# Performance work log

Hardware: AMD Instinct MI355X
Metric: run time of the kernel (lower is better)

## Reference

```python
import jax, jax.numpy as jnp
import numpy as np

B, C, H, W, NCH = 2, 256, 48, 48, 12


def setup_inputs() -> dict:
    key = jax.random.key(0)
    k1, k2, k3, k4, k5 = jax.random.split(key, 5)
    gray_feature = jax.random.normal(k1, (B, C, H, W), jnp.float32)
    rgb_feature = jax.random.normal(k2, (B, C, H, W), jnp.float32)
    rgb_image = jax.random.uniform(k3, (B, 3, H, W), jnp.float32)
    # one-hot segmentation labels: random class id per pixel in [0, NCH)
    gcls = jax.random.randint(k4, (B, H, W), 0, NCH)
    rcls = jax.random.randint(k5, (B, H, W), 0, NCH)
    gray_label = jax.nn.one_hot(gcls, NCH, axis=1, dtype=jnp.float32)
    rgb_label = jax.nn.one_hot(rcls, NCH, axis=1, dtype=jnp.float32)
    return dict(gray_feature=gray_feature, rgb_feature=rgb_feature,
                rgb_image=rgb_image, gray_label=gray_label, rgb_label=rgb_label)


def _masked_normalize(feat, maskf):
    # feat: [b,c,N], maskf: [b,N] in {0,1}. Subtract per-channel masked mean,
    # then divide each masked pixel's feature vector by its channel-norm.
    cnt = maskf.sum(-1)                                            # [b]
    mean = jnp.einsum('bcn,bn->bc', feat, maskf) / jnp.maximum(cnt, 1.0)[:, None]
    bar = (feat - mean[:, :, None]) * maskf[:, None, :]            # zero outside mask
    norm = jnp.sqrt(jnp.sum(bar * bar, axis=1))                    # [b,N]
    unit = bar / jnp.where(norm > 0, norm, 1.0)[:, None, :]
    return unit, cnt


def reference(gray_feature, rgb_feature, rgb_image, gray_label, rgb_label):
    b, c, h, w = gray_feature.shape
    N = h * w
    gf = gray_feature.reshape(b, c, N)
    rf = rgb_feature.reshape(b, c, N)
    img = rgb_image.reshape(b, 3, N)
    gms = gray_label.reshape(b, -1, N) > 0.5   # [b,NCH,N] bool
    rms = rgb_label.reshape(b, -1, N) > 0.5
    canvas = -jnp.ones((b, 3, N), gray_feature.dtype)
    NEG = jnp.asarray(-1e30, gray_feature.dtype)
    for k in range(1, 12):  # classes 1..11, matching the torch loop
        gm = gms[:, k]                                     # [b,N]
        rm = rms[:, k]
        gmf = gm.astype(gf.dtype)
        rmf = rm.astype(rf.dtype)
        gn, cg = _masked_normalize(gf, gmf)                # [b,c,N]
        rn, cr = _masked_normalize(rf, rmf)
        # normalized correlation between gray and rgb masked pixels
        corr = jnp.einsum('bci,bcj->bij', gn, rn)          # [b,N,N]
        logits = jnp.where(rm[:, None, :], corr, NEG)      # softmax over rgb-mask pixels
        sm = jax.nn.softmax(logits, axis=-1)
        out = jnp.einsum('bij,bcj->bci', sm, img)          # [b,3,N]
        # skip condition from torch: needs >=2 pixels on each side
        valid = (cg > 1) & (cr > 1)                        # [b]
        write = gm & valid[:, None]                        # [b,N]
        canvas = jnp.where(write[:, None, :], out, canvas)
    return canvas.reshape(b, 3, h, w)
```

## Files before the change

### kernel.cpp

```cpp
#include <hip/hip_runtime.h>
#include <math.h>

#define BN 2
#define CC 256
#define NN 2304
#define KK 12
#define MC 320
#define QT 16
#define KTL 256
#define KCH 32
#define BPAD 260
#define APAD 18
#define KB_ACT 11

#define OFF_CNT_G   0
#define OFF_CNT_R   32
#define OFF_IDX_G   64
#define OFF_CPS_G   (OFF_IDX_G + BN * KK * MC)
#define OFF_CPS_R   (OFF_CPS_G + BN * NN)
#define OFF_MSUM_G  (OFF_CPS_R + BN * NN)
#define OFF_MSUM_R  (OFF_MSUM_G + BN * KK * CC)
#define OFF_IMGC    (OFF_MSUM_R + BN * KK * CC)
#define OFF_INV_G   (OFF_IMGC + BN * KK * 3 * MC)
#define OFF_INV_R   (OFF_INV_G + BN * KK * MC)
#define OFF_UCG     (OFF_INV_R + BN * KK * MC)
#define OFF_UCR     (OFF_UCG + BN * KK * MC * CC)

__global__ __launch_bounds__(256) void prep_mean_kernel(
        const float* __restrict__ gf, const float* __restrict__ rf,
        const float* __restrict__ img, const float* __restrict__ gl,
        const float* __restrict__ rl, float* __restrict__ out,
        int* cnt_g, int* cnt_r, int* idx_g, int* cps_g, int* cps_r,
        float* imgc, float* inv_g, float* inv_r,
        float* msum_g, float* msum_r) {
    __shared__ int wcnt[4];
    __shared__ float wsum[4][4][KK];
    int bid = blockIdx.x, tid = threadIdx.x;
    int lane = tid & 63, wid = tid >> 6;

    if (bid < 48) {
        int type = bid / (BN * KK);
        int rem = bid % (BN * KK);
        int b = rem / KK, k = rem % KK;
        const float* lp = (type ? rl : gl) + ((size_t)(b * KK + k)) * NN;
        int* cps = type ? cps_r : cps_g;
        int* cnt = type ? cnt_r : cnt_g;
        int base = 0;
        for (int c0 = 0; c0 < NN; c0 += 256) {
            int i = c0 + tid;
            bool p = lp[i] > 0.5f;
            unsigned long long m = __ballot(p);
            int rank = __popcll(m & ((1ull << lane) - 1));
            if (lane == 0) wcnt[wid] = __popcll(m);
            __syncthreads();
            int pre = 0;
            for (int w = 0; w < wid; ++w) pre += wcnt[w];
            int tot = wcnt[0] + wcnt[1] + wcnt[2] + wcnt[3];
            if (p) {
                int pos = base + pre + rank;
                cps[b * NN + i] = (k << 16) | pos;
                if (pos < MC) {
                    if (type) {
                        for (int ch = 0; ch < 3; ++ch)
                            imgc[((b * KK + k) * 3 + ch) * MC + pos] =
                                img[((size_t)(b * 3 + ch)) * NN + i];
                    } else {
                        idx_g[(b * KK + k) * MC + pos] = i;
                    }
                }
            }
            base += tot;
            __syncthreads();
        }
        if (tid == 0) cnt[b * KK + k] = base;
        int start = base < MC ? base : MC;
        for (int pos = start + tid; pos < MC; pos += 256) {
            if (type) {
                for (int ch = 0; ch < 3; ++ch)
                    imgc[((b * KK + k) * 3 + ch) * MC + pos] = 0.f;
            } else {
                idx_g[(b * KK + k) * MC + pos] = 0;
            }
        }
        float* invc = type ? inv_r : inv_g;
        for (int pos = tid; pos < MC; pos += 256)
            invc[(b * KK + k) * MC + pos] = 0.f;
    } else {
        int u = bid - 48;
        if (u < 54) out[u * 256 + tid] = -1.0f;
        int type = u >> 7;
        int rem = u & 127;
        int b = rem >> 6, cg = rem & 63;
        const float* fb = (type ? rf : gf) + ((size_t)(b * CC + cg * 4)) * NN;
        const float* lab = (type ? rl : gl) + ((size_t)b) * KK * NN;
        float* msum = type ? msum_r : msum_g;

        float acc[4][KK];
        #pragma unroll
        for (int c = 0; c < 4; ++c)
            #pragma unroll
            for (int kk = 0; kk < KK; ++kk) acc[c][kk] = 0.f;
        for (int i = tid; i < NN; i += 256) {
            float lv[KK];
            #pragma unroll
            for (int kk = 0; kk < KK; ++kk) lv[kk] = lab[(size_t)kk * NN + i];
            #pragma unroll
            for (int c = 0; c < 4; ++c) {
                float v = fb[(size_t)c * NN + i];
                #pragma unroll
                for (int kk = 0; kk < KK; ++kk) acc[c][kk] += lv[kk] * v;
            }
        }
        #pragma unroll
        for (int c = 0; c < 4; ++c)
            #pragma unroll
            for (int kk = 0; kk < KK; ++kk) {
                #pragma unroll
                for (int o = 32; o; o >>= 1)
                    acc[c][kk] += __shfl_xor(acc[c][kk], o, 64);
            }
        if (lane == 0) {
            #pragma unroll
            for (int c = 0; c < 4; ++c)
                #pragma unroll
                for (int kk = 0; kk < KK; ++kk) wsum[wid][c][kk] = acc[c][kk];
        }
        __syncthreads();
        if (tid < 48) {
            int c = tid / KK, kk = tid % KK;
            float s = wsum[0][c][kk] + wsum[1][c][kk] + wsum[2][c][kk] + wsum[3][c][kk];
            msum[(b * KK + kk) * CC + cg * 4 + c] = s;
        }
    }
}

__global__ __launch_bounds__(256) void center_kernel(
        const float* __restrict__ gf, const float* __restrict__ rf,
        const int* __restrict__ cps_g, const int* __restrict__ cps_r,
        const int* __restrict__ cnt_g, const int* __restrict__ cnt_r,
        const float* __restrict__ msum_g, const float* __restrict__ msum_r,
        float* ucg, float* ucr, float* inv_g, float* inv_r) {
    const int PCH = NN / 32;
    int blk = blockIdx.x;
    int type = blk / (BN * PCH);
    int rem = blk % (BN * PCH);
    int b = rem / PCH, chunk = rem % PCH;
    int i0 = chunk * 32;
    const float* f = type ? rf : gf;
    const int* cps = type ? cps_r : cps_g;
    const int* cnt = type ? cnt_r : cnt_g;
    const float* msum = type ? msum_r : msum_g;
    float* uc = type ? ucr : ucg;
    float* invc = type ? inv_r : inv_g;

    __shared__ float lmean[KK * 257];
    __shared__ float tile[64 * 33];

    int tid = threadIdx.x;
    int pl = tid & 31, cb = tid >> 5;

    float r[8];
    #pragma unroll
    for (int j = 0; j < 8; ++j)
        r[j] = f[((size_t)(b * CC + cb * 8 + j)) * NN + i0 + pl];

    for (int x = tid; x < KK * CC; x += 256) {
        int k = x >> 8, c = x & 255;
        float cn = fmaxf((float)cnt[b * KK + k], 1.f);
        lmean[k * 257 + c] = msum[(b * KK + k) * CC + c] / cn;
    }
    int p = tid >> 3, q = tid & 7;
    int kcpos = cps[b * NN + i0 + p];
    int kc = kcpos >> 16, pos = kcpos & 0xFFFF;
    bool wr = pos < MC;
    float ss = 0.f;
    float* ub = uc + ((size_t)((b * KK + kc) * MC + (wr ? pos : MC - 1))) * CC;
    for (int cc = 0; cc < 4; ++cc) {
        __syncthreads();
        #pragma unroll
        for (int j = 0; j < 8; ++j)
            tile[(cb * 8 + j) * 33 + pl] = r[j];
        if (cc < 3) {
            #pragma unroll
            for (int j = 0; j < 8; ++j)
                r[j] = f[((size_t)(b * CC + (cc + 1) * 64 + cb * 8 + j)) * NN + i0 + pl];
        }
        __syncthreads();
        #pragma unroll
        for (int h = 0; h < 2; ++h) {
            int c0 = q * 8 + h * 4;
            float4 v;
            v.x = tile[(c0 + 0) * 33 + p] - lmean[kc * 257 + cc * 64 + c0 + 0];
            v.y = tile[(c0 + 1) * 33 + p] - lmean[kc * 257 + cc * 64 + c0 + 1];
            v.z = tile[(c0 + 2) * 33 + p] - lmean[kc * 257 + cc * 64 + c0 + 2];
            v.w = tile[(c0 + 3) * 33 + p] - lmean[kc * 257 + cc * 64 + c0 + 3];
            ss += v.x * v.x + v.y * v.y + v.z * v.z + v.w * v.w;
            if (wr) *(float4*)&ub[cc * 64 + c0] = v;
        }
    }
    ss += __shfl_xor(ss, 1, 64);
    ss += __shfl_xor(ss, 2, 64);
    ss += __shfl_xor(ss, 4, 64);
    if (q == 0 && wr)
        invc[(b * KK + kc) * MC + pos] = (ss > 0.f) ? rsqrtf(ss) : 1.0f;
}

__global__ __launch_bounds__(512) void corr_out_kernel(
        const int* __restrict__ cnt_g, const int* __restrict__ cnt_r,
        const int* __restrict__ idx_g,
        const float* __restrict__ ucg, const float* __restrict__ ucr,
        const float* __restrict__ inv_g, const float* __restrict__ inv_r,
        const float* __restrict__ imgc, float* __restrict__ out) {
    const int TNQ = MC / QT;
    const int NWG = BN * KB_ACT * TNQ;
    int bid = blockIdx.x;
    int x = (bid & 7) * (NWG / 8) + (bid >> 3);
    int tq = x % TNQ;
    int rest = x / TNQ;
    int k = 1 + rest % KB_ACT;
    int b = rest / KB_ACT;
    int bk = b * KK + k;
    int cg_ = cnt_g[bk], cr_ = cnt_r[bk];
    if (cg_ <= 1 || cr_ <= 1) return;
    int Mg = min(cg_, MC), Mr = min(cr_, MC);
    int q0 = tq * QT;
    if (q0 >= Mg) return;
    int mrp = (Mr + 3) & ~3;

    __shared__ float Af[CC * APAD];
    __shared__ float Bs[KCH * BPAD];

    int tid = threadIdx.x;
    {
        int r = tid >> 5, c32 = tid & 31;
        int rowi = q0 + r; if (rowi > MC - 1) rowi = MC - 1;
        const float* rowA = ucg + ((size_t)(bk * MC + rowi)) * CC;
        float4 v0 = *(const float4*)&rowA[c32 * 8];
        float4 v1 = *(const float4*)&rowA[c32 * 8 + 4];
        Af[(c32 * 8 + 0) * APAD + r] = v0.x;
        Af[(c32 * 8 + 1) * APAD + r] = v0.y;
        Af[(c32 * 8 + 2) * APAD + r] = v0.z;
        Af[(c32 * 8 + 3) * APAD + r] = v0.w;
        Af[(c32 * 8 + 4) * APAD + r] = v1.x;
        Af[(c32 * 8 + 5) * APAD + r] = v1.y;
        Af[(c32 * 8 + 6) * APAD + r] = v1.z;
        Af[(c32 * 8 + 7) * APAD + r] = v1.w;
    }

    int wv = tid >> 6;
    int lane = tid & 63;
    int r0 = q0 + 2 * wv;
    int r0c = (r0 > MC - 1) ? MC - 1 : r0;
    int r1c = (r0 + 1 > MC - 1) ? MC - 1 : r0 + 1;
    float invi0 = inv_g[bk * MC + r0c];
    float invi1 = inv_g[bk * MC + r1c];
    const float* im0 = imgc + (bk * 3 + 0) * MC;
    const float* im1 = imgc + (bk * 3 + 1) * MC;
    const float* im2 = imgc + (bk * 3 + 2) * MC;
    const float* ivr = inv_r + bk * MC;
    float s[2] = {0.f, 0.f}, p0[2] = {0.f, 0.f}, p1[2] = {0.f, 0.f}, p2[2] = {0.f, 0.f};

    int cj = tid & 7;
    int colg = tid >> 3;

    for (int k0 = 0; k0 < Mr; k0 += KTL) {
        float acc[2][4];
        #pragma unroll
        for (int xx = 0; xx < 2; ++xx)
            #pragma unroll
            for (int y = 0; y < 4; ++y) acc[xx][y] = 0.f;
        int lim = mrp - k0;

        bool act[4];
        int colr_[4], colw_[4];
        #pragma unroll
        for (int p8 = 0; p8 < 4; ++p8) {
            int col = colg + p8 * 64;
            act[p8] = col < lim;
            colw_[p8] = col;
            int cr2 = k0 + col; if (cr2 > MC - 1) cr2 = MC - 1;
            colr_[p8] = cr2;
        }
        float4 pre[4];
        #pragma unroll
        for (int p8 = 0; p8 < 4; ++p8)
            if (act[p8])
                pre[p8] = *(const float4*)(ucr +
                    ((size_t)(bk * MC + colr_[p8])) * CC + cj * 4);

        for (int kcc = 0; kcc < CC; kcc += KCH) {
            __syncthreads();
            #pragma unroll
            for (int p8 = 0; p8 < 4; ++p8) {
                if (act[p8]) {
                    int col = colw_[p8];
                    Bs[(cj * 4 + 0) * BPAD + col] = pre[p8].x;
                    Bs[(cj * 4 + 1) * BPAD + col] = pre[p8].y;
                    Bs[(cj * 4 + 2) * BPAD + col] = pre[p8].z;
                    Bs[(cj * 4 + 3) * BPAD + col] = pre[p8].w;
                }
            }
            if (kcc + KCH < CC) {
                #pragma unroll
                for (int p8 = 0; p8 < 4; ++p8)
                    if (act[p8])
                        pre[p8] = *(const float4*)(ucr +
                            ((size_t)(bk * MC + colr_[p8])) * CC + (kcc + KCH) + cj * 4);
            }
            __syncthreads();
            #pragma unroll
            for (int kk = 0; kk < KCH; ++kk) {
                float2 av = *(const float2*)&Af[(kcc + kk) * APAD + 2 * wv];
                float4 bv = *(const float4*)&Bs[kk * BPAD + lane * 4];
                acc[0][0] += av.x * bv.x; acc[0][1] += av.x * bv.y;
                acc[0][2] += av.x * bv.z; acc[0][3] += av.x * bv.w;
                acc[1][0] += av.y * bv.x; acc[1][1] += av.y * bv.y;
                acc[1][2] += av.y * bv.z; acc[1][3] += av.y * bv.w;
            }
        }
        int kbase = k0 + lane * 4; if (kbase > MC - 4) kbase = MC - 4;
        float4 w0 = *(const float4*)&im0[kbase];
        float4 w1 = *(const float4*)&im1[kbase];
        float4 w2 = *(const float4*)&im2[kbase];
        float4 vj = *(const float4*)&ivr[kbase];
        float wj0[4] = {w0.x, w0.y, w0.z, w0.w};
        float wj1[4] = {w1.x, w1.y, w1.z, w1.w};
        float wj2[4] = {w2.x, w2.y, w2.z, w2.w};
        float vjj[4] = {vj.x, vj.y, vj.z, vj.w};
        #pragma unroll
        for (int y = 0; y < 4; ++y) {
            int col = k0 + lane * 4 + y;
            bool ok = col < Mr;
            float e0 = ok ? __expf(acc[0][y] * invi0 * vjj[y]) : 0.f;
            float e1 = ok ? __expf(acc[1][y] * invi1 * vjj[y]) : 0.f;
            s[0] += e0; p0[0] += e0 * wj0[y]; p1[0] += e0 * wj1[y]; p2[0] += e0 * wj2[y];
            s[1] += e1; p0[1] += e1 * wj0[y]; p1[1] += e1 * wj1[y]; p2[1] += e1 * wj2[y];
        }
    }
    #pragma unroll
    for (int o = 1; o <= 32; o <<= 1) {
        #pragma unroll
        for (int xx = 0; xx < 2; ++xx) {
            s[xx]  += __shfl_xor(s[xx],  o, 64);
            p0[xx] += __shfl_xor(p0[xx], o, 64);
            p1[xx] += __shfl_xor(p1[xx], o, 64);
            p2[xx] += __shfl_xor(p2[xx], o, 64);
        }
    }
    if (lane == 0) {
        #pragma unroll
        for (int xx = 0; xx < 2; ++xx) {
            int row = q0 + 2 * wv + xx;
            if (row < Mg) {
                int gi = idx_g[bk * MC + row];
                float inv = 1.0f / s[xx];
                out[((size_t)(b * 3 + 0)) * NN + gi] = p0[xx] * inv;
                out[((size_t)(b * 3 + 1)) * NN + gi] = p1[xx] * inv;
                out[((size_t)(b * 3 + 2)) * NN + gi] = p2[xx] * inv;
            }
        }
    }
}

extern "C" void kernel_launch(void* const* d_in, const int* in_sizes, int n_in,
                              void* d_out, int out_size, void* d_ws, size_t ws_size,
                              hipStream_t stream) {
    const float* gf  = (const float*)d_in[0];
    const float* rf  = (const float*)d_in[1];
    const float* img = (const float*)d_in[2];
    const float* gl  = (const float*)d_in[3];
    const float* rl  = (const float*)d_in[4];
    float* out = (float*)d_out;
    float* ws = (float*)d_ws;

    int*   cnt_g  = (int*)(ws + OFF_CNT_G);
    int*   cnt_r  = (int*)(ws + OFF_CNT_R);
    int*   idx_g  = (int*)(ws + OFF_IDX_G);
    int*   cps_g  = (int*)(ws + OFF_CPS_G);
    int*   cps_r  = (int*)(ws + OFF_CPS_R);
    float* msum_g = ws + OFF_MSUM_G;
    float* msum_r = ws + OFF_MSUM_R;
    float* imgc   = ws + OFF_IMGC;
    float* inv_g  = ws + OFF_INV_G;
    float* inv_r  = ws + OFF_INV_R;
    float* ucg    = ws + OFF_UCG;
    float* ucr    = ws + OFF_UCR;

    prep_mean_kernel<<<48 + 2 * BN * (CC / 4), 256, 0, stream>>>(
        gf, rf, img, gl, rl, out, cnt_g, cnt_r, idx_g, cps_g, cps_r,
        imgc, inv_g, inv_r, msum_g, msum_r);
    center_kernel<<<2 * BN * (NN / 32), 256, 0, stream>>>(
        gf, rf, cps_g, cps_r, cnt_g, cnt_r, msum_g, msum_r,
        ucg, ucr, inv_g, inv_r);
    corr_out_kernel<<<BN * KB_ACT * (MC / QT), 512, 0, stream>>>(
        cnt_g, cnt_r, idx_g, ucg, ucr, inv_g, inv_r, imgc, out);
}
```

Before: 113.3 us.

## Merge centering into prep kernel by expanding mean subtraction algebraically

Removes the separate center kernel and its dependency on per-class means. The prep kernel now compacts raw features per pixel chunk, computing each pixel's rank from prefix counts over the labels, and stores raw squared norms. The correlation kernel recovers centered dot products and norms by expanding (a-ma)·(b-mb) with mean terms, which are computed in spare waves during the GEMM. This saves a kernel launch and a full feature pass, at the cost of redundant prefix-count scans, extra arithmetic, an extra sync, and possible cancellation error in the expanded norms.

```diff
diff --git a/kernel.cpp b/kernel.cpp
--- a/kernel.cpp
+++ b/kernel.cpp
@@ -12,6 +12,7 @@
 #define BPAD 260
 #define APAD 18
 #define KB_ACT 11
+#define PCH 72
 
 #define OFF_CNT_G   0
 #define OFF_CNT_R   32
@@ -21,72 +22,107 @@
 #define OFF_MSUM_G  (OFF_CPS_R + BN * NN)
 #define OFF_MSUM_R  (OFF_MSUM_G + BN * KK * CC)
 #define OFF_IMGC    (OFF_MSUM_R + BN * KK * CC)
-#define OFF_INV_G   (OFF_IMGC + BN * KK * 3 * MC)
-#define OFF_INV_R   (OFF_INV_G + BN * KK * MC)
-#define OFF_UCG     (OFF_INV_R + BN * KK * MC)
+#define OFF_SQ_G    (OFF_IMGC + BN * KK * 3 * MC)
+#define OFF_SQ_R    (OFF_SQ_G + BN * KK * MC)
+#define OFF_UCG     (OFF_SQ_R + BN * KK * MC)
 #define OFF_UCR     (OFF_UCG + BN * KK * MC * CC)
 
-__global__ __launch_bounds__(256) void prep_mean_kernel(
+__global__ __launch_bounds__(256) void prep_kernel(
         const float* __restrict__ gf, const float* __restrict__ rf,
         const float* __restrict__ img, const float* __restrict__ gl,
         const float* __restrict__ rl, float* __restrict__ out,
-        int* cnt_g, int* cnt_r, int* idx_g, int* cps_g, int* cps_r,
-        float* imgc, float* inv_g, float* inv_r,
-        float* msum_g, float* msum_r) {
-    __shared__ int wcnt[4];
+        int* __restrict__ cnt_g, int* __restrict__ cnt_r,
+        int* __restrict__ idx_g, float* __restrict__ imgc,
+        float* __restrict__ sq_g, float* __restrict__ sq_r,
+        float* __restrict__ msum_g, float* __restrict__ msum_r,
+        float* __restrict__ ucg, float* __restrict__ ucr) {
+    __shared__ float tile[64 * 33];
+    __shared__ int cls[32], posl[32], pcnt[KK];
     __shared__ float wsum[4][4][KK];
+    __shared__ float wcf[4][KK];
+
     int bid = blockIdx.x, tid = threadIdx.x;
     int lane = tid & 63, wid = tid >> 6;
 
-    if (bid < 48) {
-        int type = bid / (BN * KK);
-        int rem = bid % (BN * KK);
-        int b = rem / KK, k = rem % KK;
-        const float* lp = (type ? rl : gl) + ((size_t)(b * KK + k)) * NN;
-        int* cps = type ? cps_r : cps_g;
-        int* cnt = type ? cnt_r : cnt_g;
-        int base = 0;
-        for (int c0 = 0; c0 < NN; c0 += 256) {
-            int i = c0 + tid;
-            bool p = lp[i] > 0.5f;
-            unsigned long long m = __ballot(p);
-            int rank = __popcll(m & ((1ull << lane) - 1));
-            if (lane == 0) wcnt[wid] = __popcll(m);
+    if (bid < 2 * BN * PCH) {
+        int type = bid / (BN * PCH);
+        int rem = bid % (BN * PCH);
+        int b = rem / PCH, chunk = rem % PCH;
+        int i0 = chunk * 32;
+        const float* f = type ? rf : gf;
+        const float* lab = (type ? rl : gl) + (size_t)b * KK * NN;
+        float* uc = type ? ucr : ucg;
+        float* rawsq = type ? sq_r : sq_g;
+
+        if (tid < KK) pcnt[tid] = 0;
+        for (int x = tid; x < 32 * KK; x += 256) {
+            int p = x / KK, kk = x - p * KK;
+            if (lab[(size_t)kk * NN + i0 + p] > 0.5f) cls[p] = kk;
+        }
+        int pl = tid & 31, cb = tid >> 5;
+        float r[8];
+        #pragma unroll
+        for (int j = 0; j < 8; ++j)
+            r[j] = f[((size_t)(b * CC + cb * 8 + j)) * NN + i0 + pl];
+        __syncthreads();
+        for (int kk = 0; kk < KK; ++kk) {
+            int local = 0;
+            for (int i = tid; i < i0; i += 256)
+                local += (lab[(size_t)kk * NN + i] > 0.5f) ? 1 : 0;
+            #pragma unroll
+            for (int o = 32; o; o >>= 1) local += __shfl_xor(local, o, 64);
+            if (lane == 0 && local) atomicAdd(&pcnt[kk], local);
+        }
+        __syncthreads();
+        if (tid < 32) {
+            int c = cls[tid], rk = 0;
+            for (int p2 = 0; p2 < tid; ++p2) rk += (cls[p2] == c) ? 1 : 0;
+            posl[tid] = pcnt[c] + rk;
+        }
+        __syncthreads();
+        int pp = tid >> 3, qq = tid & 7;
+        int kc = cls[pp], pos = posl[pp];
+        bool wrk = pos < MC;
+        int bkc = b * KK + kc;
+        float* ub = uc + ((size_t)(bkc * MC + (wrk ? pos : MC - 1))) * CC;
+        float ss = 0.f;
+        for (int cc = 0; cc < 4; ++cc) {
             __syncthreads();
-            int pre = 0;
-            for (int w = 0; w < wid; ++w) pre += wcnt[w];
-            int tot = wcnt[0] + wcnt[1] + wcnt[2] + wcnt[3];
-            if (p) {
-                int pos = base + pre + rank;
-                cps[b * NN + i] = (k << 16) | pos;
-                if (pos < MC) {
-                    if (type) {
-                        for (int ch = 0; ch < 3; ++ch)
-                            imgc[((b * KK + k) * 3 + ch) * MC + pos] =
-                                img[((size_t)(b * 3 + ch)) * NN + i];
-                    } else {
-                        idx_g[(b * KK + k) * MC + pos] = i;
-                    }
-                }
-            }
-            base += tot;
+            #pragma unroll
+            for (int j = 0; j < 8; ++j) tile[(cb * 8 + j) * 33 + pl] = r[j];
+            if (cc < 3) {
+                #pragma unroll
+                for (int j = 0; j < 8; ++j)
+                    r[j] = f[((size_t)(b * CC + (cc + 1) * 64 + cb * 8 + j)) * NN + i0 + pl];
+            }
             __syncthreads();
-        }
-        if (tid == 0) cnt[b * KK + k] = base;
-        int start = base < MC ? base : MC;
-        for (int pos = start + tid; pos < MC; pos += 256) {
+            #pragma unroll
+            for (int h = 0; h < 2; ++h) {
+                int c0 = qq * 8 + h * 4;
+                float4 v;
+                v.x = tile[(c0 + 0) * 33 + pp];
+                v.y = tile[(c0 + 1) * 33 + pp];
+                v.z = tile[(c0 + 2) * 33 + pp];
+                v.w = tile[(c0 + 3) * 33 + pp];
+                ss += v.x * v.x + v.y * v.y + v.z * v.z + v.w * v.w;
+                if (wrk) *(float4*)&ub[cc * 64 + c0] = v;
+            }
+        }
+        ss += __shfl_xor(ss, 1, 64);
+        ss += __shfl_xor(ss, 2, 64);
+        ss += __shfl_xor(ss, 4, 64);
+        if (qq == 0 && wrk) {
+            rawsq[bkc * MC + pos] = ss;
             if (type) {
                 for (int ch = 0; ch < 3; ++ch)
-                    imgc[((b * KK + k) * 3 + ch) * MC + pos] = 0.f;
+                    imgc[(bkc * 3 + ch) * MC + pos] =
+                        img[((size_t)(b * 3 + ch)) * NN + i0 + pp];
             } else {
-                idx_g[(b * KK + k) * MC + pos] = 0;
-            }
-        }
-        float* invc = type ? inv_r : inv_g;
-        for (int pos = tid; pos < MC; pos += 256)
-            invc[(b * KK + k) * MC + pos] = 0.f;
+                idx_g[bkc * MC + pos] = i0 + pp;
+            }
+        }
     } else {
-        int u = bid - 48;
+        int u = bid - 2 * BN * PCH;
         if (u < 54) out[u * 256 + tid] = -1.0f;
         int type = u >> 7;
         int rem = u & 127;
@@ -96,14 +132,21 @@
         float* msum = type ? msum_r : msum_g;
 
         float acc[4][KK];
+        float lc[KK];
         #pragma unroll
         for (int c = 0; c < 4; ++c)
             #pragma unroll
             for (int kk = 0; kk < KK; ++kk) acc[c][kk] = 0.f;
+        #pragma unroll
+        for (int kk = 0; kk < KK; ++kk) lc[kk] = 0.f;
         for (int i = tid; i < NN; i += 256) {
             float lv[KK];
             #pragma unroll
             for (int kk = 0; kk < KK; ++kk) lv[kk] = lab[(size_t)kk * NN + i];
+            if (cg == 0) {
+                #pragma unroll
+                for (int kk = 0; kk < KK; ++kk) lc[kk] += lv[kk];
+            }
             #pragma unroll
             for (int c = 0; c < 4; ++c) {
                 float v = fb[(size_t)c * NN + i];
@@ -119,6 +162,17 @@
                 for (int o = 32; o; o >>= 1)
                     acc[c][kk] += __shfl_xor(acc[c][kk], o, 64);
             }
+        if (cg == 0) {
+            #pragma unroll
+            for (int kk = 0; kk < KK; ++kk) {
+                #pragma unroll
+                for (int o = 32; o; o >>= 1) lc[kk] += __shfl_xor(lc[kk], o, 64);
+            }
+            if (lane == 0) {
+                #pragma unroll
+                for (int kk = 0; kk < KK; ++kk) wcf[wid][kk] = lc[kk];
+            }
+        }
         if (lane == 0) {
             #pragma unroll
             for (int c = 0; c < 4; ++c)
@@ -131,85 +185,20 @@
             float s = wsum[0][c][kk] + wsum[1][c][kk] + wsum[2][c][kk] + wsum[3][c][kk];
             msum[(b * KK + kk) * CC + cg * 4 + c] = s;
         }
-    }
-}
-
-__global__ __launch_bounds__(256) void center_kernel(
-        const float* __restrict__ gf, const float* __restrict__ rf,
-        const int* __restrict__ cps_g, const int* __restrict__ cps_r,
-        const int* __restrict__ cnt_g, const int* __restrict__ cnt_r,
-        const float* __restrict__ msum_g, const float* __restrict__ msum_r,
-        float* ucg, float* ucr, float* inv_g, float* inv_r) {
-    const int PCH = NN / 32;
-    int blk = blockIdx.x;
-    int type = blk / (BN * PCH);
-    int rem = blk % (BN * PCH);
-    int b = rem / PCH, chunk = rem % PCH;
-    int i0 = chunk * 32;
-    const float* f = type ? rf : gf;
-    const int* cps = type ? cps_r : cps_g;
-    const int* cnt = type ? cnt_r : cnt_g;
-    const float* msum = type ? msum_r : msum_g;
-    float* uc = type ? ucr : ucg;
-    float* invc = type ? inv_r : inv_g;
-
-    __shared__ float lmean[KK * 257];
-    __shared__ float tile[64 * 33];
-
-    int tid = threadIdx.x;
-    int pl = tid & 31, cb = tid >> 5;
-
-    float r[8];
-    #pragma unroll
-    for (int j = 0; j < 8; ++j)
-        r[j] = f[((size_t)(b * CC + cb * 8 + j)) * NN + i0 + pl];
-
-    for (int x = tid; x < KK * CC; x += 256) {
-        int k = x >> 8, c = x & 255;
-        float cn = fmaxf((float)cnt[b * KK + k], 1.f);
-        lmean[k * 257 + c] = msum[(b * KK + k) * CC + c] / cn;
-    }
-    int p = tid >> 3, q = tid & 7;
-    int kcpos = cps[b * NN + i0 + p];
-    int kc = kcpos >> 16, pos = kcpos & 0xFFFF;
-    bool wr = pos < MC;
-    float ss = 0.f;
-    float* ub = uc + ((size_t)((b * KK + kc) * MC + (wr ? pos : MC - 1))) * CC;
-    for (int cc = 0; cc < 4; ++cc) {
-        __syncthreads();
-        #pragma unroll
-        for (int j = 0; j < 8; ++j)
-            tile[(cb * 8 + j) * 33 + pl] = r[j];
-        if (cc < 3) {
-            #pragma unroll
-            for (int j = 0; j < 8; ++j)
-                r[j] = f[((size_t)(b * CC + (cc + 1) * 64 + cb * 8 + j)) * NN + i0 + pl];
-        }
-        __syncthreads();
-        #pragma unroll
-        for (int h = 0; h < 2; ++h) {
-            int c0 = q * 8 + h * 4;
-            float4 v;
-            v.x = tile[(c0 + 0) * 33 + p] - lmean[kc * 257 + cc * 64 + c0 + 0];
-            v.y = tile[(c0 + 1) * 33 + p] - lmean[kc * 257 + cc * 64 + c0 + 1];
-            v.z = tile[(c0 + 2) * 33 + p] - lmean[kc * 257 + cc * 64 + c0 + 2];
-            v.w = tile[(c0 + 3) * 33 + p] - lmean[kc * 257 + cc * 64 + c0 + 3];
-            ss += v.x * v.x + v.y * v.y + v.z * v.z + v.w * v.w;
-            if (wr) *(float4*)&ub[cc * 64 + c0] = v;
-        }
-    }
-    ss += __shfl_xor(ss, 1, 64);
-    ss += __shfl_xor(ss, 2, 64);
-    ss += __shfl_xor(ss, 4, 64);
-    if (q == 0 && wr)
-        invc[(b * KK + kc) * MC + pos] = (ss > 0.f) ? rsqrtf(ss) : 1.0f;
+        if (cg == 0 && tid < KK) {
+            float s = wcf[0][tid] + wcf[1][tid] + wcf[2][tid] + wcf[3][tid];
+            int* cnt = type ? cnt_r : cnt_g;
+            cnt[b * KK + tid] = (int)(s + 0.5f);
+        }
+    }
 }
 
 __global__ __launch_bounds__(512) void corr_out_kernel(
         const int* __restrict__ cnt_g, const int* __restrict__ cnt_r,
         const int* __restrict__ idx_g,
         const float* __restrict__ ucg, const float* __restrict__ ucr,
-        const float* __restrict__ inv_g, const float* __restrict__ inv_r,
+        const float* __restrict__ msum_g, const float* __restrict__ msum_r,
+        const float* __restrict__ sq_g, const float* __restrict__ sq_r,
         const float* __restrict__ imgc, float* __restrict__ out) {
     const int TNQ = MC / QT;
     const int NWG = BN * KB_ACT * TNQ;
@@ -229,8 +218,12 @@
 
     __shared__ float Af[CC * APAD];
     __shared__ float Bs[KCH * BPAD];
+    __shared__ float tns[4 * 256];
+    __shared__ float ma_s[CC], mb_s[CC];
 
     int tid = threadIdx.x;
+    if (tid < 256) ma_s[tid] = msum_g[bk * CC + tid] / (float)cg_;
+    else { int c = tid - 256; mb_s[c] = msum_r[bk * CC + c] / (float)cr_; }
     {
         int r = tid >> 5, c32 = tid & 31;
         int rowi = q0 + r; if (rowi > MC - 1) rowi = MC - 1;
@@ -246,18 +239,53 @@
         Af[(c32 * 8 + 6) * APAD + r] = v1.z;
         Af[(c32 * 8 + 7) * APAD + r] = v1.w;
     }
+    __syncthreads();
 
     int wv = tid >> 6;
     int lane = tid & 63;
+
+    float vv = 0.f, na2 = 0.f, nb2 = 0.f;
+    #pragma unroll
+    for (int m = 0; m < 4; ++m) {
+        float a = ma_s[lane + 64 * m], bb = mb_s[lane + 64 * m];
+        vv += a * bb; na2 += a * a; nb2 += bb * bb;
+    }
+    #pragma unroll
+    for (int o = 32; o; o >>= 1) {
+        vv += __shfl_xor(vv, o, 64);
+        na2 += __shfl_xor(na2, o, 64);
+        nb2 += __shfl_xor(nb2, o, 64);
+    }
     int r0 = q0 + 2 * wv;
     int r0c = (r0 > MC - 1) ? MC - 1 : r0;
     int r1c = (r0 + 1 > MC - 1) ? MC - 1 : r0 + 1;
-    float invi0 = inv_g[bk * MC + r0c];
-    float invi1 = inv_g[bk * MC + r1c];
+    float wi[2], ui[2];
+    #pragma unroll
+    for (int xx = 0; xx < 2; ++xx) {
+        float s2 = 0.f, s3 = 0.f;
+        int rloc = 2 * wv + xx;
+        #pragma unroll
+        for (int m = 0; m < 4; ++m) {
+            int c = lane + 64 * m;
+            float av = Af[c * APAD + rloc];
+            s2 += av * ma_s[c]; s3 += av * mb_s[c];
+        }
+        #pragma unroll
+        for (int o = 32; o; o >>= 1) {
+            s2 += __shfl_xor(s2, o, 64);
+            s3 += __shfl_xor(s3, o, 64);
+        }
+        wi[xx] = s2; ui[xx] = s3;
+    }
+    float di0 = sq_g[bk * MC + r0c] - 2.f * wi[0] + na2;
+    float di1 = sq_g[bk * MC + r1c] - 2.f * wi[1] + na2;
+    float invi0 = di0 > 0.f ? rsqrtf(di0) : 1.f;
+    float invi1 = di1 > 0.f ? rsqrtf(di1) : 1.f;
+
     const float* im0 = imgc + (bk * 3 + 0) * MC;
     const float* im1 = imgc + (bk * 3 + 1) * MC;
     const float* im2 = imgc + (bk * 3 + 2) * MC;
-    const float* ivr = inv_r + bk * MC;
+    const float* sqr = sq_r + bk * MC;
     float s[2] = {0.f, 0.f}, p0[2] = {0.f, 0.f}, p1[2] = {0.f, 0.f}, p2[2] = {0.f, 0.f};
 
     int cj = tid & 7;
@@ -265,6 +293,7 @@
 
     for (int k0 = 0; k0 < Mr; k0 += KTL) {
         float acc[2][4];
+        float tn[4] = {0.f, 0.f, 0.f, 0.f};
         #pragma unroll
         for (int xx = 0; xx < 2; ++xx)
             #pragma unroll
@@ -308,31 +337,60 @@
                             ((size_t)(bk * MC + colr_[p8])) * CC + (kcc + KCH) + cj * 4);
             }
             __syncthreads();
-            #pragma unroll
-            for (int kk = 0; kk < KCH; ++kk) {
-                float2 av = *(const float2*)&Af[(kcc + kk) * APAD + 2 * wv];
-                float4 bv = *(const float4*)&Bs[kk * BPAD + lane * 4];
-                acc[0][0] += av.x * bv.x; acc[0][1] += av.x * bv.y;
-                acc[0][2] += av.x * bv.z; acc[0][3] += av.x * bv.w;
-                acc[1][0] += av.y * bv.x; acc[1][1] += av.y * bv.y;
-                acc[1][2] += av.y * bv.z; acc[1][3] += av.y * bv.w;
-            }
-        }
+            bool ext = (wv < 4) && ((wv & 1) == ((kcc >> 5) & 1));
+            if (ext) {
+                const float* ms = (wv >> 1) ? mb_s : ma_s;
+                #pragma unroll
+                for (int kk = 0; kk < KCH; ++kk) {
+                    float2 av = *(const float2*)&Af[(kcc + kk) * APAD + 2 * wv];
+                    float4 bv = *(const float4*)&Bs[kk * BPAD + lane * 4];
+                    float mv = ms[kcc + kk];
+                    acc[0][0] += av.x * bv.x; acc[0][1] += av.x * bv.y;
+                    acc[0][2] += av.x * bv.z; acc[0][3] += av.x * bv.w;
+                    acc[1][0] += av.y * bv.x; acc[1][1] += av.y * bv.y;
+                    acc[1][2] += av.y * bv.z; acc[1][3] += av.y * bv.w;
+                    tn[0] += mv * bv.x; tn[1] += mv * bv.y;
+                    tn[2] += mv * bv.z; tn[3] += mv * bv.w;
+                }
+            } else {
+                #pragma unroll
+                for (int kk = 0; kk < KCH; ++kk) {
+                    float2 av = *(const float2*)&Af[(kcc + kk) * APAD + 2 * wv];
+                    float4 bv = *(const float4*)&Bs[kk * BPAD + lane * 4];
+                    acc[0][0] += av.x * bv.x; acc[0][1] += av.x * bv.y;
+                    acc[0][2] += av.x * bv.z; acc[0][3] += av.x * bv.w;
+                    acc[1][0] += av.y * bv.x; acc[1][1] += av.y * bv.y;
+                    acc[1][2] += av.y * bv.z; acc[1][3] += av.y * bv.w;
+                }
+            }
+        }
+        if (wv < 4) {
+            float* dst = tns + wv * 256 + lane * 4;
+            dst[0] = tn[0]; dst[1] = tn[1]; dst[2] = tn[2]; dst[3] = tn[3];
+        }
+        __syncthreads();
         int kbase = k0 + lane * 4; if (kbase > MC - 4) kbase = MC - 4;
         float4 w0 = *(const float4*)&im0[kbase];
         float4 w1 = *(const float4*)&im1[kbase];
         float4 w2 = *(const float4*)&im2[kbase];
-        float4 vj = *(const float4*)&ivr[kbase];
+        float4 q4 = *(const float4*)&sqr[kbase];
         float wj0[4] = {w0.x, w0.y, w0.z, w0.w};
         float wj1[4] = {w1.x, w1.y, w1.z, w1.w};
         float wj2[4] = {w2.x, w2.y, w2.z, w2.w};
-        float vjj[4] = {vj.x, vj.y, vj.z, vj.w};
+        float qj[4] = {q4.x, q4.y, q4.z, q4.w};
         #pragma unroll
         for (int y = 0; y < 4; ++y) {
             int col = k0 + lane * 4 + y;
             bool ok = col < Mr;
-            float e0 = ok ? __expf(acc[0][y] * invi0 * vjj[y]) : 0.f;
-            float e1 = ok ? __expf(acc[1][y] * invi1 * vjj[y]) : 0.f;
+            int lc = lane * 4 + y;
+            float tt = tns[lc] + tns[256 + lc];
+            float nn = tns[512 + lc] + tns[768 + lc];
+            float dj = qj[y] - 2.f * nn + nb2;
+            float invj = dj > 0.f ? rsqrtf(dj) : 1.f;
+            float l0 = (acc[0][y] - ui[0] - tt + vv) * (invi0 * invj);
+            float l1 = (acc[1][y] - ui[1] - tt + vv) * (invi1 * invj);
+            float e0 = ok ? __expf(l0) : 0.f;
+            float e1 = ok ? __expf(l1) : 0.f;
             s[0] += e0; p0[0] += e0 * wj0[y]; p1[0] += e0 * wj1[y]; p2[0] += e0 * wj2[y];
             s[1] += e1; p0[1] += e1 * wj0[y]; p1[1] += e1 * wj1[y]; p2[1] += e1 * wj2[y];
         }
@@ -376,22 +434,17 @@
     int*   cnt_g  = (int*)(ws + OFF_CNT_G);
     int*   cnt_r  = (int*)(ws + OFF_CNT_R);
     int*   idx_g  = (int*)(ws + OFF_IDX_G);
-    int*   cps_g  = (int*)(ws + OFF_CPS_G);
-    int*   cps_r  = (int*)(ws + OFF_CPS_R);
     float* msum_g = ws + OFF_MSUM_G;
     float* msum_r = ws + OFF_MSUM_R;
     float* imgc   = ws + OFF_IMGC;
-    float* inv_g  = ws + OFF_INV_G;
-    float* inv_r  = ws + OFF_INV_R;
+    float* sq_g   = ws + OFF_SQ_G;
+    float* sq_r   = ws + OFF_SQ_R;
     float* ucg    = ws + OFF_UCG;
     float* ucr    = ws + OFF_UCR;
 
-    prep_mean_kernel<<<48 + 2 * BN * (CC / 4), 256, 0, stream>>>(
-        gf, rf, img, gl, rl, out, cnt_g, cnt_r, idx_g, cps_g, cps_r,
-        imgc, inv_g, inv_r, msum_g, msum_r);
-    center_kernel<<<2 * BN * (NN / 32), 256, 0, stream>>>(
-        gf, rf, cps_g, cps_r, cnt_g, cnt_r, msum_g, msum_r,
-        ucg, ucr, inv_g, inv_r);
+    prep_kernel<<<2 * BN * PCH + 256, 256, 0, stream>>>(
+        gf, rf, img, gl, rl, out, cnt_g, cnt_r, idx_g,
+        imgc, sq_g, sq_r, msum_g, msum_r, ucg, ucr);
     corr_out_kernel<<<BN * KB_ACT * (MC / QT), 512, 0, stream>>>(
-        cnt_g, cnt_r, idx_g, ucg, ucr, inv_g, inv_r, imgc, out);
+        cnt_g, cnt_r, idx_g, ucg, ucr, msum_g, msum_r, sq_g, sq_r, imgc, out);
 }
```

Result: slower. 131.1 us (+15.8%).
